# Kernel tuning notes

Hardware: AMD Instinct MI355X
Metric: run time of the kernel (lower is better)

## Reference

```python
import jax, jax.numpy as jnp
import numpy as np

LN_EPS = 1e-5

def _conv1d(x, w, b):
    # x: [B, T, Cin], w: [Cout, Cin, K] (torch layout), pad=1 -> same length for K=3
    y = jax.lax.conv_general_dilated(
        x, jnp.transpose(w, (2, 1, 0)), window_strides=(1,), padding=[(1, 1)],
        dimension_numbers=('NWC', 'WIO', 'NWC'))
    return y + b

def _layernorm(x, g, b):
    mu = jnp.mean(x, axis=-1, keepdims=True)
    var = jnp.mean(jnp.square(x - mu), axis=-1, keepdims=True)
    return (x - mu) * jax.lax.rsqrt(var + LN_EPS) * g + b

def _duration_predictor(enc, mask, w1, b1, g1, beta1, w2, b2, g2, beta2, wl, bl):
    x = enc * mask                                  # [B,T,C]
    x = _layernorm(jax.nn.relu(_conv1d(x, w1, b1)), g1, beta1)
    x = _layernorm(jax.nn.relu(_conv1d(x, w2, b2)), g2, beta2)
    out = x @ wl.T + bl                             # [B,T,1]
    return (out * mask)[..., 0]                     # [B,T]

def _expand_one(enc_i, dur_i, M):
    # enc_i: [T,C], dur_i: [T] int; fused repeat_interleave via searchsorted gather
    cs = jnp.cumsum(dur_i)                          # [T]
    pos = jnp.arange(M)                             # [M]
    idx = jnp.searchsorted(cs, pos, side='right')   # token index for each frame
    valid = pos < cs[-1]
    out = jnp.where(valid[:, None], enc_i[jnp.clip(idx, 0, enc_i.shape[0] - 1)], 0.0)
    dec = jnp.where(valid, pos + 1, 0)
    return out, dec

def setup_inputs() -> dict:
    key = jax.random.key(0)
    ks = jax.random.split(key, 12)
    B, T, C, F, M = 32, 512, 384, 384, 2048
    s = lambda n: 1.0 / np.sqrt(n)
    return {
        'encoder_output': jax.random.normal(ks[0], (B, T, C), jnp.float32),
        'encoder_output_mask': jnp.ones((B, T, 1), jnp.float32),
        'target': jax.random.randint(ks[1], (B, T), 0, 8, jnp.int32),
        'mel_max_length': M,
        'w1': jax.random.normal(ks[2], (F, C, 3), jnp.float32) * s(C * 3),
        'b1': jnp.zeros((F,), jnp.float32),
        'g1': jnp.ones((F,), jnp.float32),
        'beta1': jnp.zeros((F,), jnp.float32),
        'w2': jax.random.normal(ks[3], (F, F, 3), jnp.float32) * s(F * 3),
        'b2': jnp.zeros((F,), jnp.float32),
        'g2': jnp.ones((F,), jnp.float32),
        'beta2': jnp.zeros((F,), jnp.float32),
        'wl': jax.random.normal(ks[4], (1, F), jnp.float32) * s(F),
        'bl': jnp.zeros((1,), jnp.float32),
    }

def reference(encoder_output, encoder_output_mask, target, mel_max_length,
              w1, b1, g1, beta1, w2, b2, g2, beta2, wl, bl):
    # training-mode forward: durations come from `target`, alpha=1.0
    dpo = _duration_predictor(encoder_output, encoder_output_mask,
                              w1, b1, g1, beta1, w2, b2, g2, beta2, wl, bl)
    repeats = jnp.round(target.astype(jnp.float32) * 1.0).astype(jnp.int32)
    output, dec_pos = jax.vmap(lambda e, d: _expand_one(e, d, mel_max_length))(
        encoder_output, repeats)
    return output, dec_pos, dpo
```

## Files before the change

kernel.cpp:

```cpp
#include <hip/hip_runtime.h>
#include <hip/hip_bf16.h>
#include <stdint.h>

#define B_ 32
#define T_ 512
#define C_ 384
#define F_ 384
#define M_ 2048
#define KTOT (3 * C_)

typedef __bf16 bf16x8 __attribute__((ext_vector_type(8)));
typedef float  f32x4  __attribute__((ext_vector_type(4)));
typedef unsigned short ushort_t;

__device__ __forceinline__ ushort_t f2bf(float f) {
  __hip_bfloat16 h = __float2bfloat16(f);
  return *reinterpret_cast<ushort_t*>(&h);
}
__device__ __forceinline__ uint32_t pack2(float a, float b) {
  return (uint32_t)f2bf(a) | ((uint32_t)f2bf(b) << 16);
}

#define NWB 3456
__global__ __launch_bounds__(256) void prep_kernel(
    const int* __restrict__ target,
    const float* __restrict__ w1, const float* __restrict__ w2,
    ushort_t* __restrict__ wt1, ushort_t* __restrict__ wt2,
    int* __restrict__ cs) {
  const int gid = blockIdx.x;
  const int tid = threadIdx.x;
  if (gid < NWB) {
    int idx = gid * 256 + tid;
    int w = idx >= F_ * KTOT;
    int o = idx - (w ? F_ * KTOT : 0);
    int n = o / KTOT, k = o - n * KTOT;
    int kk = k / C_, c = k - kk * C_;
    int s = kk * 6 + (c >> 6);
    int c64 = c & 63;
    int ks = c64 >> 5, qq = (c64 >> 3) & 3, e = c64 & 7;
    int wv = n / 48, rn = n - wv * 48, fn = rn >> 4, r16 = rn & 15;
    int lane = qq * 16 + r16;
    size_t dst = ((((size_t)s * 8 + wv) * 6 + fn * 2 + ks) << 9) + lane * 8 + e;
    const float* src = w ? w2 : w1;
    (w ? wt2 : wt1)[dst] = f2bf(src[(n * C_ + c) * 3 + kk]);
  } else {
    int b = (gid - NWB) * 4 + (tid >> 6);
    int lane = tid & 63;
    int base = b * T_ + lane * 8;
    int v[8];
#pragma unroll
    for (int i = 0; i < 8; ++i) v[i] = target[base + i];
#pragma unroll
    for (int i = 1; i < 8; ++i) v[i] += v[i - 1];
    int tot = v[7];
    int inc = tot;
#pragma unroll
    for (int d = 1; d < 64; d <<= 1) {
      int t = __shfl_up(inc, d);
      if (lane >= d) inc += t;
    }
    int excl = inc - tot;
#pragma unroll
    for (int i = 0; i < 8; ++i) cs[base + i] = v[i] + excl;
  }
}

__global__ __launch_bounds__(512, 1) void gemm12_kernel(
    const float* __restrict__ enc,
    const float* __restrict__ mask,
    const ushort_t* __restrict__ wt1,
    const ushort_t* __restrict__ wt2,
    const float* __restrict__ b1, const float* __restrict__ g1,
    const float* __restrict__ be1,
    const float* __restrict__ b2, const float* __restrict__ g2,
    const float* __restrict__ be2,
    const float* __restrict__ wl, const float* __restrict__ bl,
    float* __restrict__ dpo) {
  __shared__ char ldsX[82 * 768];
  __shared__ float red[8][80][2];
  __shared__ float stats[80][2];

  const int tid = threadIdx.x;
  const int l = tid & 63, q = l >> 4, r16 = l & 15;
  const int wid = tid >> 6;
  const int b = blockIdx.x >> 3, t0 = (blockIdx.x & 7) * 64;

#pragma unroll
  for (int ps = 0; ps < 8; ++ps) {
    int idx = ps * 512 + tid;
    if (idx < 82 * 48) {
      int rl = idx / 48, cp = idx - rl * 48;
      int gc = cp >> 3, ch = cp & 7;
      int t = t0 - 2 + rl;
      uint4 o = make_uint4(0, 0, 0, 0);
      if (t >= 0 && t < T_) {
        const float* src = enc + ((size_t)b * T_ + t) * C_ + gc * 64 + ch * 8;
        float4 u = *(const float4*)src;
        float4 v = *(const float4*)(src + 4);
        float m = mask[b * T_ + t];
        o = make_uint4(pack2(u.x * m, u.y * m), pack2(u.z * m, u.w * m),
                       pack2(v.x * m, v.y * m), pack2(v.z * m, v.w * m));
      }
      *(uint4*)(ldsX + rl * 768 + gc * 128 + ((ch ^ (rl & 7)) << 4)) = o;
    }
  }

  f32x4 acc1[3][5];
#pragma unroll
  for (int fn = 0; fn < 3; ++fn)
#pragma unroll
    for (int fm = 0; fm < 5; ++fm) acc1[fn][fm] = (f32x4){0.f, 0.f, 0.f, 0.f};

  const ushort_t* wlane1 = wt1 + ((size_t)wid * 6 << 9) + (l << 3);
  const ushort_t* wlane2 = wt2 + ((size_t)wid * 6 << 9) + (l << 3);
  auto LOADW = [&](const ushort_t* wlane, bf16x8 (&dst)[3][2], int s) {
    const ushort_t* p = wlane + (((size_t)s * 48) << 9);
#pragma unroll
    for (int fn = 0; fn < 3; ++fn)
#pragma unroll
      for (int ks = 0; ks < 2; ++ks)
        dst[fn][ks] = *(const bf16x8*)(p + ((fn * 2 + ks) << 9));
  };
  auto COMP1 = [&](bf16x8 (&af)[3][2], int s) {
    const int kk = s / 6, c128 = (s % 6) * 128;
#pragma unroll
    for (int ks = 0; ks < 2; ++ks) {
      bf16x8 bx[5];
#pragma unroll
      for (int fm = 0; fm < 5; ++fm) {
        int rl = fm * 16 + r16 + kk;
        bx[fm] = *(const bf16x8*)(ldsX + rl * 768 + c128 +
                                  (((ks * 4 + q) ^ (rl & 7)) << 4));
      }
#pragma unroll
      for (int fn = 0; fn < 3; ++fn)
#pragma unroll
        for (int fm = 0; fm < 5; ++fm)
          acc1[fn][fm] = __builtin_amdgcn_mfma_f32_16x16x32_bf16(
              af[fn][ks], bx[fm], acc1[fn][fm], 0, 0, 0);
    }
  };

  {
    bf16x8 afA[3][2], afB[3][2];
    LOADW(wlane1, afA, 0);
    __syncthreads();
#pragma unroll 1
    for (int s = 0; s < 18; s += 2) {
      LOADW(wlane1, afB, s + 1);
      COMP1(afA, s);
      if (s + 2 < 18) LOADW(wlane1, afA, s + 2);
      COMP1(afB, s + 1);
    }
  }

#pragma unroll
  for (int fn = 0; fn < 3; ++fn) {
    const int nb = wid * 48 + fn * 16 + q * 4;
    float c0 = b1[nb], c1 = b1[nb + 1], c2 = b1[nb + 2], c3 = b1[nb + 3];
#pragma unroll
    for (int fm = 0; fm < 5; ++fm) {
      acc1[fn][fm][0] = fmaxf(acc1[fn][fm][0] + c0, 0.f);
      acc1[fn][fm][1] = fmaxf(acc1[fn][fm][1] + c1, 0.f);
      acc1[fn][fm][2] = fmaxf(acc1[fn][fm][2] + c2, 0.f);
      acc1[fn][fm][3] = fmaxf(acc1[fn][fm][3] + c3, 0.f);
    }
  }
#pragma unroll
  for (int fm = 0; fm < 5; ++fm) {
    float s = 0.f, s2 = 0.f;
#pragma unroll
    for (int fn = 0; fn < 3; ++fn)
#pragma unroll
      for (int j = 0; j < 4; ++j) {
        float v = acc1[fn][fm][j];
        s += v; s2 += v * v;
      }
    s += __shfl_xor(s, 16); s += __shfl_xor(s, 32);
    s2 += __shfl_xor(s2, 16); s2 += __shfl_xor(s2, 32);
    if (l < 16) { red[wid][fm * 16 + r16][0] = s; red[wid][fm * 16 + r16][1] = s2; }
  }
  __syncthreads();
  if (tid < 66) {
    float S = 0.f, S2 = 0.f;
#pragma unroll
    for (int w = 0; w < 8; ++w) { S += red[w][tid][0]; S2 += red[w][tid][1]; }
    float mu = S / F_;
    stats[tid][0] = mu;
    stats[tid][1] = rsqrtf(S2 / F_ - mu * mu + 1e-5f);
  }
  __syncthreads();

#pragma unroll
  for (int fn = 0; fn < 3; ++fn) {
    const int nb = wid * 48 + fn * 16 + q * 4;
    float g0 = g1[nb], gg1 = g1[nb + 1], g2v = g1[nb + 2], g3 = g1[nb + 3];
    float e0 = be1[nb], e1 = be1[nb + 1], e2 = be1[nb + 2], e3 = be1[nb + 3];
#pragma unroll
    for (int fm = 0; fm < 5; ++fm) {
      const int m = fm * 16 + r16;
      if (m < 66) {
        const float mu = stats[m][0], rs = stats[m][1];
        uint32_t p0 = pack2((acc1[fn][fm][0] - mu) * rs * g0 + e0,
                            (acc1[fn][fm][1] - mu) * rs * gg1 + e1);
        uint32_t p1 = pack2((acc1[fn][fm][2] - mu) * rs * g2v + e2,
                            (acc1[fn][fm][3] - mu) * rs * g3 + e3);
        *(uint2*)(ldsX + m * 768 + (((nb >> 3) ^ (m & 7)) << 4) +
                  ((q & 1) << 3)) = make_uint2(p0, p1);
      }
    }
  }
  if (t0 == 0 && tid < 48)
    *(uint4*)(ldsX + tid * 16) = make_uint4(0, 0, 0, 0);
  if (t0 == T_ - 64 && tid < 48)
    *(uint4*)(ldsX + 65 * 768 + tid * 16) = make_uint4(0, 0, 0, 0);

  f32x4 acc2[3][4];
#pragma unroll
  for (int fn = 0; fn < 3; ++fn)
#pragma unroll
    for (int fm = 0; fm < 4; ++fm) acc2[fn][fm] = (f32x4){0.f, 0.f, 0.f, 0.f};

  auto COMP2 = [&](bf16x8 (&af)[3][2], int s) {
    const int kk = s / 6, c128 = (s % 6) * 128;
#pragma unroll
    for (int ks = 0; ks < 2; ++ks) {
      bf16x8 bx[4];
#pragma unroll
      for (int fm = 0; fm < 4; ++fm) {
        int rl = fm * 16 + r16 + kk;
        bx[fm] = *(const bf16x8*)(ldsX + rl * 768 + c128 +
                                  (((ks * 4 + q) ^ (rl & 7)) << 4));
      }
#pragma unroll
      for (int fn = 0; fn < 3; ++fn)
#pragma unroll
        for (int fm = 0; fm < 4; ++fm)
          acc2[fn][fm] = __builtin_amdgcn_mfma_f32_16x16x32_bf16(
              af[fn][ks], bx[fm], acc2[fn][fm], 0, 0, 0);
    }
  };

  {
    bf16x8 afA[3][2], afB[3][2];
    LOADW(wlane2, afA, 0);
    __syncthreads();
#pragma unroll 1
    for (int s = 0; s < 18; s += 2) {
      LOADW(wlane2, afB, s + 1);
      COMP2(afA, s);
      if (s + 2 < 18) LOADW(wlane2, afA, s + 2);
      COMP2(afB, s + 1);
    }
  }

#pragma unroll
  for (int fn = 0; fn < 3; ++fn) {
    const int nb = wid * 48 + fn * 16 + q * 4;
    float c0 = b2[nb], c1 = b2[nb + 1], c2 = b2[nb + 2], c3 = b2[nb + 3];
#pragma unroll
    for (int fm = 0; fm < 4; ++fm) {
      acc2[fn][fm][0] = fmaxf(acc2[fn][fm][0] + c0, 0.f);
      acc2[fn][fm][1] = fmaxf(acc2[fn][fm][1] + c1, 0.f);
      acc2[fn][fm][2] = fmaxf(acc2[fn][fm][2] + c2, 0.f);
      acc2[fn][fm][3] = fmaxf(acc2[fn][fm][3] + c3, 0.f);
    }
  }
  __syncthreads();
#pragma unroll
  for (int fm = 0; fm < 4; ++fm) {
    float s = 0.f, s2 = 0.f;
#pragma unroll
    for (int fn = 0; fn < 3; ++fn)
#pragma unroll
      for (int j = 0; j < 4; ++j) {
        float v = acc2[fn][fm][j];
        s += v; s2 += v * v;
      }
    s += __shfl_xor(s, 16); s += __shfl_xor(s, 32);
    s2 += __shfl_xor(s2, 16); s2 += __shfl_xor(s2, 32);
    if (l < 16) { red[wid][fm * 16 + r16][0] = s; red[wid][fm * 16 + r16][1] = s2; }
  }
  __syncthreads();
  if (tid < 64) {
    float S = 0.f, S2 = 0.f;
#pragma unroll
    for (int w = 0; w < 8; ++w) { S += red[w][tid][0]; S2 += red[w][tid][1]; }
    float mu = S / F_;
    stats[tid][0] = mu;
    stats[tid][1] = rsqrtf(S2 / F_ - mu * mu + 1e-5f);
  }
  __syncthreads();

  float p[4] = {0.f, 0.f, 0.f, 0.f};
#pragma unroll
  for (int fn = 0; fn < 3; ++fn) {
    const int nb = wid * 48 + fn * 16 + q * 4;
    float g0 = g2[nb], gg1 = g2[nb + 1], g2v = g2[nb + 2], g3 = g2[nb + 3];
    float e0 = be2[nb], e1 = be2[nb + 1], e2 = be2[nb + 2], e3 = be2[nb + 3];
    float l0 = wl[nb], l1 = wl[nb + 1], l2 = wl[nb + 2], l3 = wl[nb + 3];
#pragma unroll
    for (int fm = 0; fm < 4; ++fm) {
      const int m = fm * 16 + r16;
      const float mu = stats[m][0], rs = stats[m][1];
      p[fm] += ((acc2[fn][fm][0] - mu) * rs * g0 + e0) * l0 +
               ((acc2[fn][fm][1] - mu) * rs * gg1 + e1) * l1 +
               ((acc2[fn][fm][2] - mu) * rs * g2v + e2) * l2 +
               ((acc2[fn][fm][3] - mu) * rs * g3 + e3) * l3;
    }
  }
  __syncthreads();
#pragma unroll
  for (int fm = 0; fm < 4; ++fm) {
    float s = p[fm];
    s += __shfl_xor(s, 16); s += __shfl_xor(s, 32);
    if (l < 16) red[wid][fm * 16 + r16][0] = s;
  }
  __syncthreads();
  if (tid < 64) {
    float S = 0.f;
#pragma unroll
    for (int w = 0; w < 8; ++w) S += red[w][tid][0];
    int t = t0 + tid;
    dpo[b * T_ + t] = (S + bl[0]) * mask[b * T_ + t];
  }
}

__global__ __launch_bounds__(256) void expand_kernel(
    const float* __restrict__ enc,
    const int* __restrict__ cs,
    float* __restrict__ out,
    float* __restrict__ dec) {
  __shared__ int scs[T_];
  const int blk = blockIdx.x;
  const int b = blk / (M_ / 4);
  const int p0 = (blk - b * (M_ / 4)) * 4;
  for (int i = threadIdx.x; i < T_; i += 256) scs[i] = cs[b * T_ + i];
  __syncthreads();

  const int lane = threadIdx.x & 63;
  const int wid = threadIdx.x >> 6;
  const int pos = p0 + wid;
  const int total = scs[T_ - 1];
  const bool valid = pos < total;

  int idx = 0;
#pragma unroll
  for (int step = 512; step; step >>= 1)
    if (idx + step <= T_ && scs[idx + step - 1] <= pos) idx += step;
  int src = idx < T_ ? idx : T_ - 1;

  const float4* srow = (const float4*)(enc + ((size_t)b * T_ + src) * C_);
  float4* orow = (float4*)(out + ((size_t)b * M_ + pos) * C_);
  const float4 zero = make_float4(0.f, 0.f, 0.f, 0.f);
#pragma unroll
  for (int j = 0; j < 2; ++j) {
    int c4 = j * 64 + lane;
    if (c4 < C_ / 4) orow[c4] = valid ? srow[c4] : zero;
  }
  if (lane == 0) dec[b * M_ + pos] = valid ? (float)(pos + 1) : 0.f;
}

extern "C" void kernel_launch(void* const* d_in, const int* in_sizes, int n_in,
                              void* d_out, int out_size, void* d_ws,
                              size_t ws_size, hipStream_t stream) {
  const float* enc    = (const float*)d_in[0];
  const float* mask   = (const float*)d_in[1];
  const int*   target = (const int*)d_in[2];
  const float* w1    = (const float*)d_in[4];
  const float* b1    = (const float*)d_in[5];
  const float* g1    = (const float*)d_in[6];
  const float* beta1 = (const float*)d_in[7];
  const float* w2    = (const float*)d_in[8];
  const float* b2    = (const float*)d_in[9];
  const float* g2    = (const float*)d_in[10];
  const float* beta2 = (const float*)d_in[11];
  const float* wl    = (const float*)d_in[12];
  const float* bl    = (const float*)d_in[13];

  ushort_t* wt1 = (ushort_t*)d_ws;
  ushort_t* wt2 = wt1 + (size_t)F_ * KTOT;
  int*      cs  = (int*)(wt2 + (size_t)F_ * KTOT);

  float* out0 = (float*)d_out;
  float* dec  = out0 + (size_t)B_ * M_ * C_;
  float* dpo  = dec + (size_t)B_ * M_;

  prep_kernel<<<NWB + 8, 256, 0, stream>>>(target, w1, w2, wt1, wt2, cs);

  gemm12_kernel<<<256, 512, 0, stream>>>(
      enc, mask, wt1, wt2, b1, g1, beta1, b2, g2, beta2, wl, bl, dpo);

  expand_kernel<<<(B_ * M_) / 4, 256, 0, stream>>>(enc, cs, out0, dec);
}
```

Baseline: 75.97 us.

## Fuse length-regulator expansion into the conv/layernorm GEMM kernel

Removes the separate expand kernel and appends the repeat-interleave gather to the tail of the fused duration-predictor kernel. Each of the 256 blocks reuses its LDS to hold the batch's cumulative durations and writes 256 output frames with one wave per frame. This saves a kernel launch and its launch gap. In exchange the large memory-bound copy now runs on only 256 blocks of 512 threads, with occupancy capped by the GEMM's launch bounds, which may limit memory-level parallelism. It also skips writing the padded boundary rows, since those are zeroed separately anyway.

New measurement: 80.23 us. +5.6%, slower.

```diff
diff --git a/kernel.cpp b/kernel.cpp
--- a/kernel.cpp
+++ b/kernel.cpp
@@ -75,7 +75,10 @@
     const float* __restrict__ b2, const float* __restrict__ g2,
     const float* __restrict__ be2,
     const float* __restrict__ wl, const float* __restrict__ bl,
-    float* __restrict__ dpo) {
+    float* __restrict__ dpo,
+    const int* __restrict__ cs,
+    float* __restrict__ out0,
+    float* __restrict__ dec) {
   __shared__ char ldsX[82 * 768];
   __shared__ float red[8][80][2];
   __shared__ float stats[80][2];
@@ -191,6 +194,8 @@
   }
   __syncthreads();
 
+  const int mlo = (t0 == 0) ? 1 : 0;
+  const int mhi = (t0 == T_ - 64) ? 65 : 66;
 #pragma unroll
   for (int fn = 0; fn < 3; ++fn) {
     const int nb = wid * 48 + fn * 16 + q * 4;
@@ -199,7 +204,7 @@
 #pragma unroll
     for (int fm = 0; fm < 5; ++fm) {
       const int m = fm * 16 + r16;
-      if (m < 66) {
+      if (m >= mlo && m < mhi) {
         const float mu = stats[m][0], rs = stats[m][1];
         uint32_t p0 = pack2((acc1[fn][fm][0] - mu) * rs * g0 + e0,
                             (acc1[fn][fm][1] - mu) * rs * gg1 + e1);
@@ -292,73 +297,65 @@
   }
   __syncthreads();
 
-  float p[4] = {0.f, 0.f, 0.f, 0.f};
-#pragma unroll
-  for (int fn = 0; fn < 3; ++fn) {
-    const int nb = wid * 48 + fn * 16 + q * 4;
-    float g0 = g2[nb], gg1 = g2[nb + 1], g2v = g2[nb + 2], g3 = g2[nb + 3];
-    float e0 = be2[nb], e1 = be2[nb + 1], e2 = be2[nb + 2], e3 = be2[nb + 3];
-    float l0 = wl[nb], l1 = wl[nb + 1], l2 = wl[nb + 2], l3 = wl[nb + 3];
+  {
+    float p[4] = {0.f, 0.f, 0.f, 0.f};
+#pragma unroll
+    for (int fn = 0; fn < 3; ++fn) {
+      const int nb = wid * 48 + fn * 16 + q * 4;
+      float g0 = g2[nb], gg1 = g2[nb + 1], g2v = g2[nb + 2], g3 = g2[nb + 3];
+      float e0 = be2[nb], e1 = be2[nb + 1], e2 = be2[nb + 2], e3 = be2[nb + 3];
+      float l0 = wl[nb], l1 = wl[nb + 1], l2 = wl[nb + 2], l3 = wl[nb + 3];
+#pragma unroll
+      for (int fm = 0; fm < 4; ++fm) {
+        const int m = fm * 16 + r16;
+        const float mu = stats[m][0], rs = stats[m][1];
+        p[fm] += ((acc2[fn][fm][0] - mu) * rs * g0 + e0) * l0 +
+                 ((acc2[fn][fm][1] - mu) * rs * gg1 + e1) * l1 +
+                 ((acc2[fn][fm][2] - mu) * rs * g2v + e2) * l2 +
+                 ((acc2[fn][fm][3] - mu) * rs * g3 + e3) * l3;
+      }
+    }
+    __syncthreads();
 #pragma unroll
     for (int fm = 0; fm < 4; ++fm) {
-      const int m = fm * 16 + r16;
-      const float mu = stats[m][0], rs = stats[m][1];
-      p[fm] += ((acc2[fn][fm][0] - mu) * rs * g0 + e0) * l0 +
-               ((acc2[fn][fm][1] - mu) * rs * gg1 + e1) * l1 +
-               ((acc2[fn][fm][2] - mu) * rs * g2v + e2) * l2 +
-               ((acc2[fn][fm][3] - mu) * rs * g3 + e3) * l3;
-    }
-  }
-  __syncthreads();
-#pragma unroll
-  for (int fm = 0; fm < 4; ++fm) {
-    float s = p[fm];
-    s += __shfl_xor(s, 16); s += __shfl_xor(s, 32);
-    if (l < 16) red[wid][fm * 16 + r16][0] = s;
-  }
-  __syncthreads();
-  if (tid < 64) {
-    float S = 0.f;
-#pragma unroll
-    for (int w = 0; w < 8; ++w) S += red[w][tid][0];
-    int t = t0 + tid;
-    dpo[b * T_ + t] = (S + bl[0]) * mask[b * T_ + t];
-  }
-}
-
-__global__ __launch_bounds__(256) void expand_kernel(
-    const float* __restrict__ enc,
-    const int* __restrict__ cs,
-    float* __restrict__ out,
-    float* __restrict__ dec) {
-  __shared__ int scs[T_];
-  const int blk = blockIdx.x;
-  const int b = blk / (M_ / 4);
-  const int p0 = (blk - b * (M_ / 4)) * 4;
-  for (int i = threadIdx.x; i < T_; i += 256) scs[i] = cs[b * T_ + i];
-  __syncthreads();
-
-  const int lane = threadIdx.x & 63;
-  const int wid = threadIdx.x >> 6;
-  const int pos = p0 + wid;
-  const int total = scs[T_ - 1];
-  const bool valid = pos < total;
-
-  int idx = 0;
-#pragma unroll
-  for (int step = 512; step; step >>= 1)
-    if (idx + step <= T_ && scs[idx + step - 1] <= pos) idx += step;
-  int src = idx < T_ ? idx : T_ - 1;
-
-  const float4* srow = (const float4*)(enc + ((size_t)b * T_ + src) * C_);
-  float4* orow = (float4*)(out + ((size_t)b * M_ + pos) * C_);
-  const float4 zero = make_float4(0.f, 0.f, 0.f, 0.f);
-#pragma unroll
-  for (int j = 0; j < 2; ++j) {
-    int c4 = j * 64 + lane;
-    if (c4 < C_ / 4) orow[c4] = valid ? srow[c4] : zero;
-  }
-  if (lane == 0) dec[b * M_ + pos] = valid ? (float)(pos + 1) : 0.f;
+      float s = p[fm];
+      s += __shfl_xor(s, 16); s += __shfl_xor(s, 32);
+      if (l < 16) red[wid][fm * 16 + r16][0] = s;
+    }
+    __syncthreads();
+    if (tid < 64) {
+      float S = 0.f;
+#pragma unroll
+      for (int w = 0; w < 8; ++w) S += red[w][tid][0];
+      int t = t0 + tid;
+      dpo[b * T_ + t] = (S + bl[0]) * mask[b * T_ + t];
+    }
+  }
+
+  __syncthreads();
+  {
+    int* scs = (int*)ldsX;
+    for (int i = tid; i < T_; i += 512) scs[i] = cs[b * T_ + i];
+    __syncthreads();
+    const int total = scs[T_ - 1];
+    const int p0 = (blockIdx.x & 7) * 256;
+    const float4 zero = make_float4(0.f, 0.f, 0.f, 0.f);
+#pragma unroll 1
+    for (int it = 0; it < 32; ++it) {
+      const int pos = p0 + it * 8 + wid;
+      const bool valid = pos < total;
+      int idx = 0;
+#pragma unroll
+      for (int step = 512; step; step >>= 1)
+        if (idx + step <= T_ && scs[idx + step - 1] <= pos) idx += step;
+      int src = idx < T_ ? idx : T_ - 1;
+      const float4* srow = (const float4*)(enc + ((size_t)b * T_ + src) * C_);
+      float4* orow = (float4*)(out0 + ((size_t)b * M_ + pos) * C_);
+      orow[l] = valid ? srow[l] : zero;
+      if (l < 32) orow[64 + l] = valid ? srow[64 + l] : zero;
+      if (l == 0) dec[b * M_ + pos] = valid ? (float)(pos + 1) : 0.f;
+    }
+  }
 }
 
 extern "C" void kernel_launch(void* const* d_in, const int* in_sizes, int n_in,
@@ -389,7 +386,6 @@
   prep_kernel<<<NWB + 8, 256, 0, stream>>>(target, w1, w2, wt1, wt2, cs);
 
   gemm12_kernel<<<256, 512, 0, stream>>>(
-      enc, mask, wt1, wt2, b1, g1, beta1, b2, g2, beta2, wl, bl, dpo);
-
-  expand_kernel<<<(B_ * M_) / 4, 256, 0, stream>>>(enc, cs, out0, dec);
-}
+      enc, mask, wt1, wt2, b1, g1, beta1, b2, g2, beta2, wl, bl, dpo,
+      cs, out0, dec);
+}
```

## Fuse length-regulator expansion into weight-prep kernel and drop cumsum buffer

Applied to the files above, without the earlier changes.

The separate expand kernel is merged into the weight-prep kernel. Each expansion block now computes its batch's prefix sum of durations in shared memory and writes 16 output frames, instead of reading a global cumsum buffer written by an earlier block. This removes one kernel launch and the global cumsum round trip, and lets the bandwidth-heavy expansion overlap with the bf16 weight conversion before the GEMM kernel runs. The cumsum is recomputed in all 4096 expansion blocks, and the GEMM kernel now starts only after the expansion writes are finished. A minor tweak also skips writing boundary rows in the GEMM LDS stage, since those rows are zeroed anyway.

Measured after the change: 65.49 us. 1.16x faster.

```diff
diff --git a/kernel.cpp b/kernel.cpp
--- a/kernel.cpp
+++ b/kernel.cpp
@@ -22,11 +22,14 @@
 }
 
 #define NWB 3456
-__global__ __launch_bounds__(256) void prep_kernel(
+#define NEXB 4096
+__global__ __launch_bounds__(256) void prep_expand_kernel(
     const int* __restrict__ target,
     const float* __restrict__ w1, const float* __restrict__ w2,
+    const float* __restrict__ enc,
     ushort_t* __restrict__ wt1, ushort_t* __restrict__ wt2,
-    int* __restrict__ cs) {
+    float* __restrict__ out0,
+    float* __restrict__ dec) {
   const int gid = blockIdx.x;
   const int tid = threadIdx.x;
   if (gid < NWB) {
@@ -43,9 +46,15 @@
     size_t dst = ((((size_t)s * 8 + wv) * 6 + fn * 2 + ks) << 9) + lane * 8 + e;
     const float* src = w ? w2 : w1;
     (w ? wt2 : wt1)[dst] = f2bf(src[(n * C_ + c) * 3 + kk]);
-  } else {
-    int b = (gid - NWB) * 4 + (tid >> 6);
-    int lane = tid & 63;
+    return;
+  }
+
+  __shared__ int scs[T_];
+  const int eb = gid - NWB;
+  const int b = eb >> 7;
+  const int p0 = (eb & 127) * 16;
+  if (tid < 64) {
+    int lane = tid;
     int base = b * T_ + lane * 8;
     int v[8];
 #pragma unroll
@@ -61,7 +70,27 @@
     }
     int excl = inc - tot;
 #pragma unroll
-    for (int i = 0; i < 8; ++i) cs[base + i] = v[i] + excl;
+    for (int i = 0; i < 8; ++i) scs[lane * 8 + i] = v[i] + excl;
+  }
+  __syncthreads();
+
+  const int lane = tid & 63, wid = tid >> 6;
+  const int total = scs[T_ - 1];
+  const float4 zero = make_float4(0.f, 0.f, 0.f, 0.f);
+#pragma unroll
+  for (int it = 0; it < 4; ++it) {
+    const int pos = p0 + it * 4 + wid;
+    const bool valid = pos < total;
+    int idx = 0;
+#pragma unroll
+    for (int step = 512; step; step >>= 1)
+      if (idx + step <= T_ && scs[idx + step - 1] <= pos) idx += step;
+    int src = idx < T_ ? idx : T_ - 1;
+    const float4* srow = (const float4*)(enc + ((size_t)b * T_ + src) * C_);
+    float4* orow = (float4*)(out0 + ((size_t)b * M_ + pos) * C_);
+    orow[lane] = valid ? srow[lane] : zero;
+    if (lane < 32) orow[64 + lane] = valid ? srow[64 + lane] : zero;
+    if (lane == 0) dec[b * M_ + pos] = valid ? (float)(pos + 1) : 0.f;
   }
 }
 
@@ -191,6 +220,8 @@
   }
   __syncthreads();
 
+  const int mlo = (t0 == 0) ? 1 : 0;
+  const int mhi = (t0 == T_ - 64) ? 65 : 66;
 #pragma unroll
   for (int fn = 0; fn < 3; ++fn) {
     const int nb = wid * 48 + fn * 16 + q * 4;
@@ -199,7 +230,7 @@
 #pragma unroll
     for (int fm = 0; fm < 5; ++fm) {
       const int m = fm * 16 + r16;
-      if (m < 66) {
+      if (m >= mlo && m < mhi) {
         const float mu = stats[m][0], rs = stats[m][1];
         uint32_t p0 = pack2((acc1[fn][fm][0] - mu) * rs * g0 + e0,
                             (acc1[fn][fm][1] - mu) * rs * gg1 + e1);
@@ -324,41 +355,6 @@
     int t = t0 + tid;
     dpo[b * T_ + t] = (S + bl[0]) * mask[b * T_ + t];
   }
-}
-
-__global__ __launch_bounds__(256) void expand_kernel(
-    const float* __restrict__ enc,
-    const int* __restrict__ cs,
-    float* __restrict__ out,
-    float* __restrict__ dec) {
-  __shared__ int scs[T_];
-  const int blk = blockIdx.x;
-  const int b = blk / (M_ / 4);
-  const int p0 = (blk - b * (M_ / 4)) * 4;
-  for (int i = threadIdx.x; i < T_; i += 256) scs[i] = cs[b * T_ + i];
-  __syncthreads();
-
-  const int lane = threadIdx.x & 63;
-  const int wid = threadIdx.x >> 6;
-  const int pos = p0 + wid;
-  const int total = scs[T_ - 1];
-  const bool valid = pos < total;
-
-  int idx = 0;
-#pragma unroll
-  for (int step = 512; step; step >>= 1)
-    if (idx + step <= T_ && scs[idx + step - 1] <= pos) idx += step;
-  int src = idx < T_ ? idx : T_ - 1;
-
-  const float4* srow = (const float4*)(enc + ((size_t)b * T_ + src) * C_);
-  float4* orow = (float4*)(out + ((size_t)b * M_ + pos) * C_);
-  const float4 zero = make_float4(0.f, 0.f, 0.f, 0.f);
-#pragma unroll
-  for (int j = 0; j < 2; ++j) {
-    int c4 = j * 64 + lane;
-    if (c4 < C_ / 4) orow[c4] = valid ? srow[c4] : zero;
-  }
-  if (lane == 0) dec[b * M_ + pos] = valid ? (float)(pos + 1) : 0.f;
 }
 
 extern "C" void kernel_launch(void* const* d_in, const int* in_sizes, int n_in,
@@ -380,16 +376,14 @@
 
   ushort_t* wt1 = (ushort_t*)d_ws;
   ushort_t* wt2 = wt1 + (size_t)F_ * KTOT;
-  int*      cs  = (int*)(wt2 + (size_t)F_ * KTOT);
 
   float* out0 = (float*)d_out;
   float* dec  = out0 + (size_t)B_ * M_ * C_;
   float* dpo  = dec + (size_t)B_ * M_;
 
-  prep_kernel<<<NWB + 8, 256, 0, stream>>>(target, w1, w2, wt1, wt2, cs);
+  prep_expand_kernel<<<NWB + NEXB, 256, 0, stream>>>(
+      target, w1, w2, enc, wt1, wt2, out0, dec);
 
   gemm12_kernel<<<256, 512, 0, stream>>>(
       enc, mask, wt1, wt2, b1, g1, beta1, b2, g2, beta2, wl, bl, dpo);
-
-  expand_kernel<<<(B_ * M_) / 4, 256, 0, stream>>>(enc, cs, out0, dec);
-}
+}
```
